# Optimization experiments

Measured on AMD Instinct MI355X. Metric: run time of the kernel, lower is better.

The kernel has to match this reference:

```python
import jax, jax.numpy as jnp
import numpy as np

B, H, W, C = 16, 64, 64, 256
NH = 8
KD = C // NH  # 32
SCALE = KD ** -0.5


def rotate_every_two(x):
    x1 = x[..., ::2]
    x2 = x[..., 1::2]
    return jnp.stack([-x2, x1], axis=-1).reshape(x.shape)


def theta_shift(x, sin, cos):
    return x * cos + rotate_every_two(x) * sin


def dwconv2d(x, w, b):
    # x: (b,h,w,c), w: (5,5,1,c) HWIO depthwise, pad 2
    y = jax.lax.conv_general_dilated(
        x, w, window_strides=(1, 1), padding=((2, 2), (2, 2)),
        dimension_numbers=("NHWC", "HWIO", "NHWC"), feature_group_count=x.shape[-1])
    return y + b


def setup_inputs() -> dict:
    key = jax.random.key(0)
    ks = jax.random.split(key, 12)
    s = 0.02
    return {
        "x": jax.random.normal(ks[0], (B, H, W, C), jnp.float32),
        "sin": jax.random.uniform(ks[1], (H, W, KD), jnp.float32, -1.0, 1.0),
        "cos": jax.random.uniform(ks[2], (H, W, KD), jnp.float32, -1.0, 1.0),
        "mask_h": jax.random.normal(ks[3], (NH, H, H), jnp.float32) * 0.1,
        "mask_w": jax.random.normal(ks[4], (NH, W, W), jnp.float32) * 0.1,
        "Wq": jax.random.normal(ks[5], (C, C), jnp.float32) * s,
        "bq": jnp.zeros((C,), jnp.float32),
        "Wk": jax.random.normal(ks[6], (C, C), jnp.float32) * s,
        "bk": jnp.zeros((C,), jnp.float32),
        "Wv": jax.random.normal(ks[7], (C, C), jnp.float32) * s,
        "bv": jnp.zeros((C,), jnp.float32),
        "conv_w": jax.random.normal(ks[8], (5, 5, 1, C), jnp.float32) * s,
        "conv_b": jnp.zeros((C,), jnp.float32),
        "Wo": jax.random.normal(ks[9], (C, C), jnp.float32) * s,
        "bo": jnp.zeros((C,), jnp.float32),
    }


def reference(x, sin, cos, mask_h, mask_w, Wq, bq, Wk, bk, Wv, bv, conv_w, conv_b, Wo, bo):
    b, h, w, _ = x.shape
    n = mask_w.shape[0]
    kd = sin.shape[-1]

    q = x @ Wq + bq
    k = (x @ Wk + bk) * SCALE
    v = x @ Wv + bv
    lepe = dwconv2d(v, conv_w, conv_b)

    # (b,n,h,w,d)
    q = q.reshape(b, h, w, n, kd).transpose(0, 3, 1, 2, 4)
    k = k.reshape(b, h, w, n, kd).transpose(0, 3, 1, 2, 4)
    qr = theta_shift(q, sin, cos)
    kr = theta_shift(k, sin, cos)

    # width attention: rows independent
    qk_w = jnp.einsum("bhnwd,bhnvd->bhnwv", qr.transpose(0, 2, 1, 3, 4), kr.transpose(0, 2, 1, 3, 4))
    qk_w = jax.nn.softmax(qk_w + mask_w, axis=-1)
    vv = v.reshape(b, h, w, n, -1).transpose(0, 1, 3, 2, 4)  # (b,h,n,w,d2)
    vv = jnp.einsum("bhnwv,bhnvd->bhnwd", qk_w, vv)

    # height attention: columns independent
    qr_h = qr.transpose(0, 3, 1, 2, 4)  # (b,w,n,h,d)
    kr_h = kr.transpose(0, 3, 1, 2, 4)
    vv = vv.transpose(0, 3, 2, 1, 4)  # (b,w,n,h,d2)
    qk_h = jnp.einsum("bwnhd,bwngd->bwnhg", qr_h, kr_h)
    qk_h = jax.nn.softmax(qk_h + mask_h, axis=-1)
    out = jnp.einsum("bwnhg,bwngd->bwnhd", qk_h, vv)

    out = out.transpose(0, 3, 1, 2, 4).reshape(b, h, w, -1)  # (b,h,w,n*d2)
    out = out + lepe
    return out @ Wo + bo
```

## Files before the change

kernel.cpp:

```cpp
#include <hip/hip_runtime.h>

typedef __attribute__((ext_vector_type(8))) short bf16x8;
typedef __attribute__((ext_vector_type(4))) float f32x4;

constexpr int B  = 16;
constexpr int H  = 64;
constexpr int W  = 64;
constexpr int C  = 256;
constexpr int NH = 8;
constexpr int KD = 32;
constexpr float SCALE = 0.17677669529663687f;
constexpr int M_TOT = B * H * W;
constexpr size_t NEL = (size_t)B * H * W * C;

__device__ __forceinline__ unsigned short f2bf(float f) {
    union { float f; unsigned int u; } x; x.f = f;
    unsigned int u = x.u;
    unsigned int r = (u + 0x7fffu + ((u >> 16) & 1u)) >> 16;
    return (unsigned short)r;
}
__device__ __forceinline__ float bf2f(unsigned short s) {
    union { unsigned int u; float f; } x; x.u = ((unsigned int)s) << 16; return x.f;
}
__device__ __forceinline__ float bf_lo(unsigned int u) {
    union { unsigned int u; float f; } x; x.u = u << 16; return x.f;
}
__device__ __forceinline__ float bf_hi(unsigned int u) {
    union { unsigned int u; float f; } x; x.u = u & 0xffff0000u; return x.f;
}
__device__ __forceinline__ unsigned int pack2(float a, float b) {
    return (unsigned int)f2bf(a) | ((unsigned int)f2bf(b) << 16);
}
__device__ __forceinline__ int swz(int row, int kp8) {
    return row * 32 + (kp8 ^ (((row >> 2) & 3) << 3));
}

typedef const __attribute__((address_space(1))) unsigned int gas_uint;
typedef __attribute__((address_space(3))) unsigned int las_uint;
__device__ __forceinline__ void gl16(const unsigned short* g, unsigned short* l) {
    __builtin_amdgcn_global_load_lds((gas_uint*)g, (las_uint*)l, 16, 0, 0);
}

__global__ __launch_bounds__(256) void prep_x16(const float* __restrict__ x,
                                                unsigned short* __restrict__ x16) {
    size_t i8 = ((size_t)blockIdx.x * 256 + threadIdx.x) * 8;
    float4 f0 = *(const float4*)(x + i8);
    float4 f1 = *(const float4*)(x + i8 + 4);
    uint4 o;
    o.x = pack2(f0.x, f0.y); o.y = pack2(f0.z, f0.w);
    o.z = pack2(f1.x, f1.y); o.w = pack2(f1.z, f1.w);
    *(uint4*)(x16 + i8) = o;
}

__global__ __launch_bounds__(256) void trans_w(const float* __restrict__ src,
                                               unsigned short* __restrict__ dst) {
    int tid = blockIdx.x * 256 + threadIdx.x;
    int n = tid >> 5, k0 = (tid & 31) << 3;
    unsigned int p[4];
#pragma unroll
    for (int j = 0; j < 4; ++j) {
        float a  = src[(size_t)(k0 + 2 * j) * 256 + n];
        float b2 = src[(size_t)(k0 + 2 * j + 1) * 256 + n];
        p[j] = pack2(a, b2);
    }
    uint4 o = {p[0], p[1], p[2], p[3]};
    *(uint4*)(dst + (size_t)n * 256 + k0) = o;
}

template <int QK>
__global__ __launch_bounds__(256) void qkv_part(
    const unsigned short* __restrict__ x16, const unsigned short* __restrict__ Wt16,
    const float* __restrict__ bq, const float* __restrict__ bk, const float* __restrict__ bv,
    const float* __restrict__ sin_t, const float* __restrict__ cos_t,
    unsigned short* __restrict__ qr, unsigned short* __restrict__ kr,
    unsigned short* __restrict__ v16)
{
    __shared__ __align__(16) unsigned short As[128 * 32];
    __shared__ __align__(16) unsigned short Bs[128 * 32];

    const int t = threadIdx.x;
    const int lane = t & 63, wid = t >> 6;
    const int wr = wid >> 1, wc = wid & 1;
    const int m0 = blockIdx.x * 128;
    const int yb = blockIdx.y;
    const int wrow0 = QK ? yb * 128 : 512 + yb * 128;
    const int nb    = QK ? (yb & 1) * 128 : yb * 128;
    const int matid = QK ? (yb >> 1) : 2;

    f32x4 acc[4][4];
#pragma unroll
    for (int i = 0; i < 4; ++i)
#pragma unroll
        for (int j = 0; j < 4; ++j)
#pragma unroll
            for (int q = 0; q < 4; ++q) acc[i][j][q] = 0.f;

    const int lco = ((lane >> 2) << 8) + (((lane & 3) ^ (lane >> 4)) << 3);
    const unsigned short* ag = x16 + (size_t)m0 * 256 + lco;
    const unsigned short* bg = Wt16 + (size_t)wrow0 * 256 + lco;
    unsigned short* al0 = As + wid * 16 * 32;
    unsigned short* al1 = As + (64 + wid * 16) * 32;
    unsigned short* bl0 = Bs + wid * 16 * 32;
    unsigned short* bl1 = Bs + (64 + wid * 16) * 32;
    const int rg0 = wid * 16 * 256, rg1 = (64 + wid * 16) * 256;

    const int rsel = lane & 15, kg8 = (lane >> 4) << 3;

    for (int ks = 0; ks < 8; ++ks) {
        const int k0 = ks * 32;
        __syncthreads();
        gl16(ag + rg0 + k0, al0);
        gl16(ag + rg1 + k0, al1);
        gl16(bg + rg0 + k0, bl0);
        gl16(bg + rg1 + k0, bl1);
        __syncthreads();

        bf16x8 af[4], bf[4];
#pragma unroll
        for (int i = 0; i < 4; ++i)
            af[i] = *(const bf16x8*)(&As[swz(wr * 64 + i * 16 + rsel, kg8)]);
#pragma unroll
        for (int j = 0; j < 4; ++j)
            bf[j] = *(const bf16x8*)(&Bs[swz(wc * 64 + j * 16 + rsel, kg8)]);
#pragma unroll
        for (int i = 0; i < 4; ++i)
#pragma unroll
            for (int j = 0; j < 4; ++j) {
                if (QK)
                    acc[i][j] = __builtin_amdgcn_mfma_f32_16x16x32_bf16(bf[j], af[i], acc[i][j], 0, 0, 0);
                else
                    acc[i][j] = __builtin_amdgcn_mfma_f32_16x16x32_bf16(af[i], bf[j], acc[i][j], 0, 0, 0);
            }
    }

    const int col_l = lane & 15, rowg = (lane >> 4) << 2;
    if (QK == 0) {
#pragma unroll
        for (int i = 0; i < 4; ++i)
#pragma unroll
            for (int j = 0; j < 4; ++j) {
                int nn = nb + wc * 64 + j * 16 + col_l;
                float bias = bv[nn];
#pragma unroll
                for (int r = 0; r < 4; ++r) {
                    int m = m0 + wr * 64 + i * 16 + rowg + r;
                    v16[(size_t)m * 256 + nn] = f2bf(acc[i][j][r] + bias);
                }
            }
    } else {
        const float sc = matid ? SCALE : 1.0f;
        const float* __restrict__ bias = matid ? bk : bq;
        unsigned short* __restrict__ dst = matid ? kr : qr;
#pragma unroll
        for (int i = 0; i < 4; ++i) {
            const int m = m0 + wr * 64 + i * 16 + col_l;
            const int bb = m >> 12, hh = (m >> 6) & 63, ww = m & 63;
            const size_t pixbase = ((size_t)hh * 64 + ww) * 32;
#pragma unroll
            for (int j = 0; j < 4; ++j) {
                const int n = nb + wc * 64 + j * 16 + rowg;
                const int nh = n >> 5, db = n & 31;
                float4 bias4 = *(const float4*)(bias + n);
                float4 cs4 = *(const float4*)(cos_t + pixbase + db);
                float4 sn4 = *(const float4*)(sin_t + pixbase + db);
                float v0 = (acc[i][j][0] + bias4.x) * sc;
                float v1 = (acc[i][j][1] + bias4.y) * sc;
                float v2 = (acc[i][j][2] + bias4.z) * sc;
                float v3 = (acc[i][j][3] + bias4.w) * sc;
                ushort4 o;
                o.x = f2bf(v0 * cs4.x - v1 * sn4.x);
                o.y = f2bf(v1 * cs4.y + v0 * sn4.y);
                o.z = f2bf(v2 * cs4.z - v3 * sn4.z);
                o.w = f2bf(v3 * cs4.w + v2 * sn4.w);
                *(ushort4*)(dst + ((((size_t)bb * 8 + nh) * 64 + hh) * 64 + ww) * 32 + db) = o;
            }
        }
    }
}

__global__ __launch_bounds__(256) void conv_kernel(
    const unsigned short* __restrict__ v, const float* __restrict__ cw,
    const float* __restrict__ cb, unsigned short* __restrict__ lepe)
{
    size_t tid = (size_t)blockIdx.x * 256 + threadIdx.x;
    const int c8 = (int)(tid & 31) << 3;
    const int w  = (int)(tid >> 5) & 63;
    const int h  = (int)(tid >> 11) & 63;
    const int b  = (int)(tid >> 17);

    float acc[8];
    {
        float4 cb0 = *(const float4*)(cb + c8);
        float4 cb1 = *(const float4*)(cb + c8 + 4);
        acc[0] = cb0.x; acc[1] = cb0.y; acc[2] = cb0.z; acc[3] = cb0.w;
        acc[4] = cb1.x; acc[5] = cb1.y; acc[6] = cb1.z; acc[7] = cb1.w;
    }

    const unsigned short* __restrict__ vb = v + (size_t)b * 4096 * 256 + c8;
#pragma unroll
    for (int dy = 0; dy < 5; ++dy) {
        int yy = h + dy - 2;
        if (yy < 0 || yy >= 64) continue;
#pragma unroll
        for (int dx = 0; dx < 5; ++dx) {
            int xx = w + dx - 2;
            if (xx < 0 || xx >= 64) continue;
            uint4 rv = *(const uint4*)(vb + (size_t)(yy * 64 + xx) * 256);
            const float* wp = cw + (dy * 5 + dx) * 256 + c8;
            float4 w0 = *(const float4*)wp;
            float4 w1 = *(const float4*)(wp + 4);
            acc[0] += bf_lo(rv.x) * w0.x; acc[1] += bf_hi(rv.x) * w0.y;
            acc[2] += bf_lo(rv.y) * w0.z; acc[3] += bf_hi(rv.y) * w0.w;
            acc[4] += bf_lo(rv.z) * w1.x; acc[5] += bf_hi(rv.z) * w1.y;
            acc[6] += bf_lo(rv.w) * w1.z; acc[7] += bf_hi(rv.w) * w1.w;
        }
    }

    uint4 ov;
    ov.x = pack2(acc[0], acc[1]); ov.y = pack2(acc[2], acc[3]);
    ov.z = pack2(acc[4], acc[5]); ov.w = pack2(acc[6], acc[7]);
    *(uint4*)(lepe + tid * 8) = ov;
}

template <int AXIS>
__global__ __launch_bounds__(256) void attn_mfma(
    const unsigned short* __restrict__ qr, const unsigned short* __restrict__ kr,
    const unsigned short* __restrict__ vin, const float* __restrict__ mask,
    const unsigned short* __restrict__ addin, unsigned short* __restrict__ outp)
{
    __shared__ __align__(16) short qs[64 * 40];
    __shared__ __align__(16) short ks[64 * 40];
    __shared__ __align__(16) short vt[32 * 72];
    __shared__ __align__(16) short P [64 * 72];

    const int t    = threadIdx.x;
    const int lane = t & 63, wv = t >> 6;
    const int bid  = blockIdx.x;
    const int nh   = bid & 7;
    const int pos  = (bid >> 3) & 63;
    const int b    = bid >> 9;

    size_t qbase, vbase;
    int qstride, vstride;
    if (AXIS == 0) {
        qbase   = ((size_t)(b * 8 + nh) * 64 + pos) * 2048;
        qstride = 32;
        vbase   = ((size_t)(b * 64 + pos) * 64) * 256 + nh * 32;
        vstride = 256;
    } else {
        qbase   = ((size_t)(b * 8 + nh) * 64) * 2048 + pos * 32;
        qstride = 2048;
        vbase   = ((size_t)b * 64 * 64) * 256 + pos * 256 + nh * 32;
        vstride = 16384;
    }

    {
        int row = t >> 2, c8 = (t & 3) << 3;
        uint4 rq = *(const uint4*)(qr + qbase + (size_t)row * qstride + c8);
        *(uint4*)(&qs[row * 40 + c8]) = rq;
        uint4 rk = *(const uint4*)(kr + qbase + (size_t)row * qstride + c8);
        *(uint4*)(&ks[row * 40 + c8]) = rk;
        uint4 rv = *(const uint4*)(vin + vbase + (size_t)row * vstride + c8);
        const unsigned short* pv = (const unsigned short*)&rv;
#pragma unroll
        for (int j = 0; j < 8; ++j) vt[(c8 + j) * 72 + row] = pv[j];
    }
    __syncthreads();

    const int rsel = lane & 15;
    const int kg   = (lane >> 4) << 3;
    const int rowg = (lane >> 4) << 2;

    bf16x8 aq = *(const bf16x8*)(&qs[(wv * 16 + rsel) * 40 + kg]);
    f32x4 s[4];
#pragma unroll
    for (int j = 0; j < 4; ++j) {
        f32x4 z = {0.f, 0.f, 0.f, 0.f};
        bf16x8 bk8 = *(const bf16x8*)(&ks[(j * 16 + rsel) * 40 + kg]);
        s[j] = __builtin_amdgcn_mfma_f32_16x16x32_bf16(aq, bk8, z, 0, 0, 0);
    }

    const float* __restrict__ mrow = mask + (size_t)nh * 4096;
#pragma unroll
    for (int r = 0; r < 4; ++r) {
        const int grow = wv * 16 + rowg + r;
#pragma unroll
        for (int j = 0; j < 4; ++j)
            s[j][r] += mrow[grow * 64 + j * 16 + rsel];
        float mx = fmaxf(fmaxf(s[0][r], s[1][r]), fmaxf(s[2][r], s[3][r]));
        mx = fmaxf(mx, __shfl_xor(mx, 1));
        mx = fmaxf(mx, __shfl_xor(mx, 2));
        mx = fmaxf(mx, __shfl_xor(mx, 4));
        mx = fmaxf(mx, __shfl_xor(mx, 8));
        float e0 = __expf(s[0][r] - mx), e1 = __expf(s[1][r] - mx);
        float e2 = __expf(s[2][r] - mx), e3 = __expf(s[3][r] - mx);
        float sum = e0 + e1 + e2 + e3;
        sum += __shfl_xor(sum, 1);
        sum += __shfl_xor(sum, 2);
        sum += __shfl_xor(sum, 4);
        sum += __shfl_xor(sum, 8);
        float inv = 1.0f / sum;
        P[grow * 72 +      rsel] = f2bf(e0 * inv);
        P[grow * 72 + 16 + rsel] = f2bf(e1 * inv);
        P[grow * 72 + 32 + rsel] = f2bf(e2 * inv);
        P[grow * 72 + 48 + rsel] = f2bf(e3 * inv);
    }
    __syncthreads();

    f32x4 o[2];
#pragma unroll
    for (int n = 0; n < 2; ++n)
#pragma unroll
        for (int q = 0; q < 4; ++q) o[n][q] = 0.f;
#pragma unroll
    for (int kk = 0; kk < 2; ++kk) {
        bf16x8 ap = *(const bf16x8*)(&P[(wv * 16 + rsel) * 72 + kk * 32 + kg]);
#pragma unroll
        for (int n = 0; n < 2; ++n) {
            bf16x8 bv8 = *(const bf16x8*)(&vt[(n * 16 + rsel) * 72 + kk * 32 + kg]);
            o[n] = __builtin_amdgcn_mfma_f32_16x16x32_bf16(ap, bv8, o[n], 0, 0, 0);
        }
    }

#pragma unroll
    for (int n = 0; n < 2; ++n)
#pragma unroll
        for (int r = 0; r < 4; ++r) {
            const int grow = wv * 16 + rowg + r;
            size_t oidx = vbase + (size_t)grow * vstride + n * 16 + rsel;
            float val = o[n][r];
            if (AXIS == 1) val += bf2f(addin[oidx]);
            outp[oidx] = f2bf(val);
        }
}

__global__ __launch_bounds__(256) void gemm_out_mfma(
    const unsigned short* __restrict__ y16, const unsigned short* __restrict__ Wot16,
    const float* __restrict__ bo, float* __restrict__ out)
{
    __shared__ __align__(16) unsigned short As[128 * 32];
    __shared__ __align__(16) unsigned short Bs[128 * 32];

    const int t = threadIdx.x;
    const int lane = t & 63, wid = t >> 6;
    const int wr = wid >> 1, wc = wid & 1;
    const int m0 = blockIdx.x * 128;
    const int n0 = blockIdx.y * 128;

    f32x4 acc[4][4];
#pragma unroll
    for (int i = 0; i < 4; ++i)
#pragma unroll
        for (int j = 0; j < 4; ++j)
#pragma unroll
            for (int q = 0; q < 4; ++q) acc[i][j][q] = 0.f;

    const int lco = ((lane >> 2) << 8) + (((lane & 3) ^ (lane >> 4)) << 3);
    const unsigned short* ag = y16 + (size_t)m0 * 256 + lco;
    const unsigned short* bg = Wot16 + (size_t)n0 * 256 + lco;
    unsigned short* al0 = As + wid * 16 * 32;
    unsigned short* al1 = As + (64 + wid * 16) * 32;
    unsigned short* bl0 = Bs + wid * 16 * 32;
    unsigned short* bl1 = Bs + (64 + wid * 16) * 32;
    const int rg0 = wid * 16 * 256, rg1 = (64 + wid * 16) * 256;

    const int rsel = lane & 15, kg8 = (lane >> 4) << 3;

    for (int ks = 0; ks < 8; ++ks) {
        const int k0 = ks * 32;
        __syncthreads();
        gl16(ag + rg0 + k0, al0);
        gl16(ag + rg1 + k0, al1);
        gl16(bg + rg0 + k0, bl0);
        gl16(bg + rg1 + k0, bl1);
        __syncthreads();

        bf16x8 af[4], bf[4];
#pragma unroll
        for (int i = 0; i < 4; ++i)
            af[i] = *(const bf16x8*)(&As[swz(wr * 64 + i * 16 + rsel, kg8)]);
#pragma unroll
        for (int j = 0; j < 4; ++j)
            bf[j] = *(const bf16x8*)(&Bs[swz(wc * 64 + j * 16 + rsel, kg8)]);
#pragma unroll
        for (int i = 0; i < 4; ++i)
#pragma unroll
            for (int j = 0; j < 4; ++j)
                acc[i][j] = __builtin_amdgcn_mfma_f32_16x16x32_bf16(af[i], bf[j], acc[i][j], 0, 0, 0);
    }

    const int col_l = lane & 15, rowg = (lane >> 4) << 2;
#pragma unroll
    for (int i = 0; i < 4; ++i)
#pragma unroll
        for (int j = 0; j < 4; ++j) {
            int nn = n0 + wc * 64 + j * 16 + col_l;
            float bias = bo[nn];
#pragma unroll
            for (int r = 0; r < 4; ++r) {
                int m = m0 + wr * 64 + i * 16 + rowg + r;
                out[(size_t)m * 256 + nn] = acc[i][j][r] + bias;
            }
        }
}

extern "C" void kernel_launch(void* const* d_in, const int* in_sizes, int n_in,
                              void* d_out, int out_size, void* d_ws, size_t ws_size,
                              hipStream_t stream) {
    const float* x      = (const float*)d_in[0];
    const float* sin_t  = (const float*)d_in[1];
    const float* cos_t  = (const float*)d_in[2];
    const float* mask_h = (const float*)d_in[3];
    const float* mask_w = (const float*)d_in[4];
    const float* Wq     = (const float*)d_in[5];
    const float* bq     = (const float*)d_in[6];
    const float* Wk     = (const float*)d_in[7];
    const float* bk     = (const float*)d_in[8];
    const float* Wv     = (const float*)d_in[9];
    const float* bv     = (const float*)d_in[10];
    const float* conv_w = (const float*)d_in[11];
    const float* conv_b = (const float*)d_in[12];
    const float* Wo     = (const float*)d_in[13];
    const float* bo     = (const float*)d_in[14];

    unsigned short* ws    = (unsigned short*)d_ws;
    unsigned short* v16   = ws;
    unsigned short* lepe16= v16 + NEL;
    unsigned short* qr16  = lepe16 + NEL;
    unsigned short* kr16  = qr16 + NEL;
    unsigned short* y16   = kr16 + NEL;
    unsigned short* Wt16  = y16 + NEL;
    unsigned short* Wot16 = Wt16 + 768 * 256;

    unsigned short* vv16 = (unsigned short*)d_out;
    unsigned short* x16  = (unsigned short*)d_out + NEL;

    prep_x16<<<(int)(NEL / 2048), 256, 0, stream>>>(x, x16);
    trans_w<<<32, 256, 0, stream>>>(Wq, Wt16);
    trans_w<<<32, 256, 0, stream>>>(Wk, Wt16 + 256 * 256);
    trans_w<<<32, 256, 0, stream>>>(Wv, Wt16 + 512 * 256);
    trans_w<<<32, 256, 0, stream>>>(Wo, Wot16);

    qkv_part<1><<<dim3(M_TOT / 128, 4), 256, 0, stream>>>(
        x16, Wt16, bq, bk, bv, sin_t, cos_t, qr16, kr16, v16);
    qkv_part<0><<<dim3(M_TOT / 128, 2), 256, 0, stream>>>(
        x16, Wt16, bq, bk, bv, sin_t, cos_t, qr16, kr16, v16);

    conv_kernel<<<(int)(NEL / 2048), 256, 0, stream>>>(v16, conv_w, conv_b, lepe16);

    attn_mfma<0><<<B * H * NH, 256, 0, stream>>>(qr16, kr16, v16, mask_w, nullptr, vv16);

    attn_mfma<1><<<B * W * NH, 256, 0, stream>>>(qr16, kr16, vv16, mask_h, lepe16, y16);

    gemm_out_mfma<<<dim3(M_TOT / 128, 2), 256, 0, stream>>>(y16, Wot16, bo, (float*)d_out);
}
```

Baseline: 275.0 us.

## Double-buffer LDS in QKV/output GEMMs and register-block depthwise conv

```diff
diff --git a/kernel.cpp b/kernel.cpp
--- a/kernel.cpp
+++ b/kernel.cpp
@@ -31,6 +31,10 @@
 __device__ __forceinline__ unsigned int pack2(float a, float b) {
     return (unsigned int)f2bf(a) | ((unsigned int)f2bf(b) << 16);
 }
+__device__ __forceinline__ void cvt8(uint4 rv, float* f) {
+    f[0] = bf_lo(rv.x); f[1] = bf_hi(rv.x); f[2] = bf_lo(rv.y); f[3] = bf_hi(rv.y);
+    f[4] = bf_lo(rv.z); f[5] = bf_hi(rv.z); f[6] = bf_lo(rv.w); f[7] = bf_hi(rv.w);
+}
 __device__ __forceinline__ int swz(int row, int kp8) {
     return row * 32 + (kp8 ^ (((row >> 2) & 3) << 3));
 }
@@ -75,8 +79,8 @@
     unsigned short* __restrict__ qr, unsigned short* __restrict__ kr,
     unsigned short* __restrict__ v16)
 {
-    __shared__ __align__(16) unsigned short As[128 * 32];
-    __shared__ __align__(16) unsigned short Bs[128 * 32];
+    __shared__ __align__(16) unsigned short As[2][128 * 32];
+    __shared__ __align__(16) unsigned short Bs[2][128 * 32];
 
     const int t = threadIdx.x;
     const int lane = t & 63, wid = t >> 6;
@@ -98,30 +102,35 @@
     const int lco = ((lane >> 2) << 8) + (((lane & 3) ^ (lane >> 4)) << 3);
     const unsigned short* ag = x16 + (size_t)m0 * 256 + lco;
     const unsigned short* bg = Wt16 + (size_t)wrow0 * 256 + lco;
-    unsigned short* al0 = As + wid * 16 * 32;
-    unsigned short* al1 = As + (64 + wid * 16) * 32;
-    unsigned short* bl0 = Bs + wid * 16 * 32;
-    unsigned short* bl1 = Bs + (64 + wid * 16) * 32;
+    const int lds0 = wid * 16 * 32;
+    const int lds1 = (64 + wid * 16) * 32;
     const int rg0 = wid * 16 * 256, rg1 = (64 + wid * 16) * 256;
 
     const int rsel = lane & 15, kg8 = (lane >> 4) << 3;
 
+    gl16(ag + rg0, &As[0][lds0]);
+    gl16(ag + rg1, &As[0][lds1]);
+    gl16(bg + rg0, &Bs[0][lds0]);
+    gl16(bg + rg1, &Bs[0][lds1]);
+    __syncthreads();
+
+    int cur = 0;
     for (int ks = 0; ks < 8; ++ks) {
-        const int k0 = ks * 32;
-        __syncthreads();
-        gl16(ag + rg0 + k0, al0);
-        gl16(ag + rg1 + k0, al1);
-        gl16(bg + rg0 + k0, bl0);
-        gl16(bg + rg1 + k0, bl1);
-        __syncthreads();
+        if (ks < 7) {
+            const int kn = (ks + 1) * 32;
+            gl16(ag + rg0 + kn, &As[cur ^ 1][lds0]);
+            gl16(ag + rg1 + kn, &As[cur ^ 1][lds1]);
+            gl16(bg + rg0 + kn, &Bs[cur ^ 1][lds0]);
+            gl16(bg + rg1 + kn, &Bs[cur ^ 1][lds1]);
+        }
 
         bf16x8 af[4], bf[4];
 #pragma unroll
         for (int i = 0; i < 4; ++i)
-            af[i] = *(const bf16x8*)(&As[swz(wr * 64 + i * 16 + rsel, kg8)]);
+            af[i] = *(const bf16x8*)(&As[cur][swz(wr * 64 + i * 16 + rsel, kg8)]);
 #pragma unroll
         for (int j = 0; j < 4; ++j)
-            bf[j] = *(const bf16x8*)(&Bs[swz(wc * 64 + j * 16 + rsel, kg8)]);
+            bf[j] = *(const bf16x8*)(&Bs[cur][swz(wc * 64 + j * 16 + rsel, kg8)]);
 #pragma unroll
         for (int i = 0; i < 4; ++i)
 #pragma unroll
@@ -131,6 +140,8 @@
                 else
                     acc[i][j] = __builtin_amdgcn_mfma_f32_16x16x32_bf16(af[i], bf[j], acc[i][j], 0, 0, 0);
             }
+        __syncthreads();
+        cur ^= 1;
     }
 
     const int col_l = lane & 15, rowg = (lane >> 4) << 2;
@@ -184,42 +195,62 @@
 {
     size_t tid = (size_t)blockIdx.x * 256 + threadIdx.x;
     const int c8 = (int)(tid & 31) << 3;
-    const int w  = (int)(tid >> 5) & 63;
-    const int h  = (int)(tid >> 11) & 63;
-    const int b  = (int)(tid >> 17);
-
-    float acc[8];
+    const int w0 = ((int)(tid >> 5) & 15) << 2;
+    const int h  = (int)(tid >> 9) & 63;
+    const int b  = (int)(tid >> 15);
+
+    float acc[4][8];
     {
         float4 cb0 = *(const float4*)(cb + c8);
         float4 cb1 = *(const float4*)(cb + c8 + 4);
-        acc[0] = cb0.x; acc[1] = cb0.y; acc[2] = cb0.z; acc[3] = cb0.w;
-        acc[4] = cb1.x; acc[5] = cb1.y; acc[6] = cb1.z; acc[7] = cb1.w;
+#pragma unroll
+        for (int o = 0; o < 4; ++o) {
+            acc[o][0] = cb0.x; acc[o][1] = cb0.y; acc[o][2] = cb0.z; acc[o][3] = cb0.w;
+            acc[o][4] = cb1.x; acc[o][5] = cb1.y; acc[o][6] = cb1.z; acc[o][7] = cb1.w;
+        }
     }
 
     const unsigned short* __restrict__ vb = v + (size_t)b * 4096 * 256 + c8;
 #pragma unroll
     for (int dy = 0; dy < 5; ++dy) {
-        int yy = h + dy - 2;
+        const int yy = h + dy - 2;
         if (yy < 0 || yy >= 64) continue;
+        float rowf[8][8];
+#pragma unroll
+        for (int j = 0; j < 8; ++j) {
+            const int xx = w0 + j - 2;
+            if (xx < 0 || xx >= 64) {
+#pragma unroll
+                for (int q = 0; q < 8; ++q) rowf[j][q] = 0.f;
+            } else {
+                uint4 rv = *(const uint4*)(vb + (size_t)(yy * 64 + xx) * 256);
+                cvt8(rv, rowf[j]);
+            }
+        }
 #pragma unroll
         for (int dx = 0; dx < 5; ++dx) {
-            int xx = w + dx - 2;
-            if (xx < 0 || xx >= 64) continue;
-            uint4 rv = *(const uint4*)(vb + (size_t)(yy * 64 + xx) * 256);
             const float* wp = cw + (dy * 5 + dx) * 256 + c8;
-            float4 w0 = *(const float4*)wp;
-            float4 w1 = *(const float4*)(wp + 4);
-            acc[0] += bf_lo(rv.x) * w0.x; acc[1] += bf_hi(rv.x) * w0.y;
-            acc[2] += bf_lo(rv.y) * w0.z; acc[3] += bf_hi(rv.y) * w0.w;
-            acc[4] += bf_lo(rv.z) * w1.x; acc[5] += bf_hi(rv.z) * w1.y;
-            acc[6] += bf_lo(rv.w) * w1.z; acc[7] += bf_hi(rv.w) * w1.w;
-        }
-    }
-
-    uint4 ov;
-    ov.x = pack2(acc[0], acc[1]); ov.y = pack2(acc[2], acc[3]);
-    ov.z = pack2(acc[4], acc[5]); ov.w = pack2(acc[6], acc[7]);
-    *(uint4*)(lepe + tid * 8) = ov;
+            float4 wv0 = *(const float4*)wp;
+            float4 wv1 = *(const float4*)(wp + 4);
+#pragma unroll
+            for (int o = 0; o < 4; ++o) {
+                const float* rf = rowf[dx + o];
+                acc[o][0] += rf[0] * wv0.x; acc[o][1] += rf[1] * wv0.y;
+                acc[o][2] += rf[2] * wv0.z; acc[o][3] += rf[3] * wv0.w;
+                acc[o][4] += rf[4] * wv1.x; acc[o][5] += rf[5] * wv1.y;
+                acc[o][6] += rf[6] * wv1.z; acc[o][7] += rf[7] * wv1.w;
+            }
+        }
+    }
+
+    unsigned short* __restrict__ op = lepe + (((size_t)(b * 64 + h) * 64) + w0) * 256 + c8;
+#pragma unroll
+    for (int o = 0; o < 4; ++o) {
+        uint4 ov;
+        ov.x = pack2(acc[o][0], acc[o][1]); ov.y = pack2(acc[o][2], acc[o][3]);
+        ov.z = pack2(acc[o][4], acc[o][5]); ov.w = pack2(acc[o][6], acc[o][7]);
+        *(uint4*)(op + (size_t)o * 256) = ov;
+    }
 }
 
 template <int AXIS>
@@ -338,8 +369,8 @@
     const unsigned short* __restrict__ y16, const unsigned short* __restrict__ Wot16,
     const float* __restrict__ bo, float* __restrict__ out)
 {
-    __shared__ __align__(16) unsigned short As[128 * 32];
-    __shared__ __align__(16) unsigned short Bs[128 * 32];
+    __shared__ __align__(16) unsigned short As[2][128 * 32];
+    __shared__ __align__(16) unsigned short Bs[2][128 * 32];
 
     const int t = threadIdx.x;
     const int lane = t & 63, wid = t >> 6;
@@ -358,35 +389,42 @@
     const int lco = ((lane >> 2) << 8) + (((lane & 3) ^ (lane >> 4)) << 3);
     const unsigned short* ag = y16 + (size_t)m0 * 256 + lco;
     const unsigned short* bg = Wot16 + (size_t)n0 * 256 + lco;
-    unsigned short* al0 = As + wid * 16 * 32;
-    unsigned short* al1 = As + (64 + wid * 16) * 32;
-    unsigned short* bl0 = Bs + wid * 16 * 32;
-    unsigned short* bl1 = Bs + (64 + wid * 16) * 32;
+    const int lds0 = wid * 16 * 32;
+    const int lds1 = (64 + wid * 16) * 32;
     const int rg0 = wid * 16 * 256, rg1 = (64 + wid * 16) * 256;
 
     const int rsel = lane & 15, kg8 = (lane >> 4) << 3;
 
+    gl16(ag + rg0, &As[0][lds0]);
+    gl16(ag + rg1, &As[0][lds1]);
+    gl16(bg + rg0, &Bs[0][lds0]);
+    gl16(bg + rg1, &Bs[0][lds1]);
+    __syncthreads();
+
+    int cur = 0;
     for (int ks = 0; ks < 8; ++ks) {
-        const int k0 = ks * 32;
-        __syncthreads();
-        gl16(ag + rg0 + k0, al0);
-        gl16(ag + rg1 + k0, al1);
-        gl16(bg + rg0 + k0, bl0);
-        gl16(bg + rg1 + k0, bl1);
-        __syncthreads();
+        if (ks < 7) {
+            const int kn = (ks + 1) * 32;
+            gl16(ag + rg0 + kn, &As[cur ^ 1][lds0]);
+            gl16(ag + rg1 + kn, &As[cur ^ 1][lds1]);
+            gl16(bg + rg0 + kn, &Bs[cur ^ 1][lds0]);
+            gl16(bg + rg1 + kn, &Bs[cur ^ 1][lds1]);
+        }
 
         bf16x8 af[4], bf[4];
 #pragma unroll
         for (int i = 0; i < 4; ++i)
-            af[i] = *(const bf16x8*)(&As[swz(wr * 64 + i * 16 + rsel, kg8)]);
+            af[i] = *(const bf16x8*)(&As[cur][swz(wr * 64 + i * 16 + rsel, kg8)]);
 #pragma unroll
         for (int j = 0; j < 4; ++j)
-            bf[j] = *(const bf16x8*)(&Bs[swz(wc * 64 + j * 16 + rsel, kg8)]);
+            bf[j] = *(const bf16x8*)(&Bs[cur][swz(wc * 64 + j * 16 + rsel, kg8)]);
 #pragma unroll
         for (int i = 0; i < 4; ++i)
 #pragma unroll
             for (int j = 0; j < 4; ++j)
                 acc[i][j] = __builtin_amdgcn_mfma_f32_16x16x32_bf16(af[i], bf[j], acc[i][j], 0, 0, 0);
+        __syncthreads();
+        cur ^= 1;
     }
 
     const int col_l = lane & 15, rowg = (lane >> 4) << 2;
@@ -446,7 +484,7 @@
     qkv_part<0><<<dim3(M_TOT / 128, 2), 256, 0, stream>>>(
         x16, Wt16, bq, bk, bv, sin_t, cos_t, qr16, kr16, v16);
 
-    conv_kernel<<<(int)(NEL / 2048), 256, 0, stream>>>(v16, conv_w, conv_b, lepe16);
+    conv_kernel<<<(int)(NEL / 32 / 256), 256, 0, stream>>>(v16, conv_w, conv_b, lepe16);
 
     attn_mfma<0><<<B * H * NH, 256, 0, stream>>>(qr16, kr16, v16, mask_w, nullptr, vv16);
 
```

Result: faster. 250.6 us (-8.9%).
